# Performance work log

Hardware: AMD Instinct MI355X
Metric: run time of the kernel (lower is better)

The kernel has to match this reference:

```python
import jax, jax.numpy as jnp
import numpy as np

N_NODES = 100000
N_EDGES = 1600000
EMBED_DIM = 64


def setup_inputs() -> dict:
    key = jax.random.key(0)
    k_x, k_e, k_w, k_b = jax.random.split(key, 4)
    x = jax.random.normal(k_x, (N_NODES, EMBED_DIM), dtype=jnp.float32)
    edge_index = jax.random.randint(k_e, (2, N_EDGES), 0, N_NODES, dtype=jnp.int64)
    # nn.Linear(embed_dim, embed_dim): weight [out, in], bias [out]
    W = jax.random.normal(k_w, (EMBED_DIM, EMBED_DIM), dtype=jnp.float32) * (1.0 / np.sqrt(EMBED_DIM))
    b = jax.random.normal(k_b, (EMBED_DIM,), dtype=jnp.float32) * 0.01
    return {"x": x, "edge_index": edge_index, "W": W, "b": b, "num_node": N_NODES}


def reference(x, edge_index, W, b, num_node):
    source_nodes, target_nodes = edge_index[0], edge_index[1]
    # h = relu(Linear(x))  -> [N, d]
    h = jax.nn.relu(jnp.einsum("nd,od->no", x, W) + b)
    # gather messages at target nodes: [E, d]
    msgs = h[target_nodes]
    # scatter-add into source node slots (index_add_)
    aggr = jax.ops.segment_sum(msgs, source_nodes, num_segments=num_node)
    # mean normalization: bincount clamped to >= 1
    counts = jnp.bincount(source_nodes, length=num_node).astype(jnp.float32)
    counts = jnp.maximum(counts, 1.0)
    # dropout is identity at inference (training=False)
    return aggr / counts[:, None]
```

## Files before the change

### kernel.cpp

```cpp
#include <hip/hip_runtime.h>
#include <hip/hip_bf16.h>

#define DIM 64
#define SCAN_B 256
#define NXCD 8

__global__ void detect_layout_kernel(const int* __restrict__ ei32,
                                     int* __restrict__ flag) {
  int v = ei32[2 * threadIdx.x + 1];
  unsigned long long m = __ballot(v != 0);
  if (threadIdx.x == 0) *flag = (m == 0ULL) ? 1 : 0;
}

__device__ __forceinline__ int load_idx(const int* ei32, int is64, size_t pos) {
  return is64 ? ei32[2 * pos] : ei32[pos];
}

__global__ __launch_bounds__(256) void linear_relu_kernel(
    const float* __restrict__ x, const float* __restrict__ W,
    const float* __restrict__ b, float* __restrict__ h, int N) {
  __shared__ float Ws[DIM * DIM];
  __shared__ float bs[DIM];
  for (int i = threadIdx.x; i < DIM * DIM; i += 256) Ws[i] = W[i];
  if (threadIdx.x < DIM) bs[threadIdx.x] = b[threadIdx.x];
  __syncthreads();

  int row = blockIdx.x * 256 + threadIdx.x;
  if (row >= N) return;

  const float4* xr = (const float4*)(x + (size_t)row * DIM);
  float acc[DIM];
#pragma unroll
  for (int o = 0; o < DIM; ++o) acc[o] = bs[o];

#pragma unroll
  for (int i4 = 0; i4 < DIM / 4; ++i4) {
    float4 xv = xr[i4];
#pragma unroll
    for (int o = 0; o < DIM; ++o) {
      const float* wrow = &Ws[o * DIM + i4 * 4];
      acc[o] = fmaf(xv.x, wrow[0], acc[o]);
      acc[o] = fmaf(xv.y, wrow[1], acc[o]);
      acc[o] = fmaf(xv.z, wrow[2], acc[o]);
      acc[o] = fmaf(xv.w, wrow[3], acc[o]);
    }
  }

  float4* hr = (float4*)(h + (size_t)row * DIM);
#pragma unroll
  for (int o4 = 0; o4 < DIM / 4; ++o4) {
    float4 v;
    v.x = fmaxf(acc[o4 * 4 + 0], 0.0f);
    v.y = fmaxf(acc[o4 * 4 + 1], 0.0f);
    v.z = fmaxf(acc[o4 * 4 + 2], 0.0f);
    v.w = fmaxf(acc[o4 * 4 + 3], 0.0f);
    hr[o4] = v;
  }
}

__global__ __launch_bounds__(256) void hist_xcd_kernel(
    const int* __restrict__ ei32, const int* __restrict__ flag,
    int* __restrict__ counts8, int* __restrict__ rank,
    int* __restrict__ chunk_xcd, int N, int E) {
  unsigned int xcc;
  asm volatile("s_getreg_b32 %0, hwreg(HW_REG_XCC_ID)" : "=s"(xcc));
  xcc &= (NXCD - 1);
  if (threadIdx.x == 0) chunk_xcd[blockIdx.x] = (int)xcc;

  int e = blockIdx.x * 256 + threadIdx.x;
  if (e >= E) return;
  int src = load_idx(ei32, *flag, (size_t)e);
  int* ctr = counts8 + (size_t)xcc * N + src;
  int r = __hip_atomic_fetch_add(ctr, 1, __ATOMIC_RELAXED,
                                 __HIP_MEMORY_SCOPE_WORKGROUP);
  __builtin_nontemporal_store(r, &rank[e]);
}

__global__ void scan1_kernel(int* __restrict__ counts8, int* __restrict__ ctot,
                             int* __restrict__ offsets,
                             int* __restrict__ partials, int N) {
  __shared__ int s[SCAN_B];
  int t = threadIdx.x;
  int i = blockIdx.x * SCAN_B + t;
  int total = 0;
  if (i < N) {
    int run = 0;
#pragma unroll
    for (int x = 0; x < NXCD; ++x) {
      size_t idx = (size_t)x * N + i;
      int c = counts8[idx];
      counts8[idx] = run;
      run += c;
    }
    total = run;
    ctot[i] = total;
  }
  s[t] = total;
  __syncthreads();
  for (int off = 1; off < SCAN_B; off <<= 1) {
    int add = (t >= off) ? s[t - off] : 0;
    __syncthreads();
    s[t] += add;
    __syncthreads();
  }
  if (i < N) offsets[i] = s[t] - total;
  if (t == SCAN_B - 1) partials[blockIdx.x] = s[t];
}

__global__ void scan2_kernel(int* __restrict__ partials, int nb) {
  __shared__ int s[512];
  int t = threadIdx.x;
  int v = (t < nb) ? partials[t] : 0;
  s[t] = v;
  __syncthreads();
  for (int off = 1; off < 512; off <<= 1) {
    int add = (t >= off) ? s[t - off] : 0;
    __syncthreads();
    s[t] += add;
    __syncthreads();
  }
  if (t < nb) partials[t] = s[t] - v;
}

__global__ void scan3_kernel(int* __restrict__ offsets,
                             const int* __restrict__ partials, int N) {
  int i = blockIdx.x * SCAN_B + threadIdx.x;
  if (i < N) offsets[i] += partials[blockIdx.x];
}

__global__ __launch_bounds__(256) void place_kernel(
    const int* __restrict__ ei32, const int* __restrict__ flag,
    const int* __restrict__ offsets, const int* __restrict__ counts8,
    const int* __restrict__ rank, const int* __restrict__ chunk_xcd,
    int* __restrict__ bucket, int N, int E) {
  int e = blockIdx.x * 256 + threadIdx.x;
  if (e >= E) return;
  int is64 = *flag;
  int xcd = chunk_xcd[blockIdx.x];
  int src = load_idx(ei32, is64, (size_t)e);
  int tgt = load_idx(ei32, is64, (size_t)E + e);
  int r = __builtin_nontemporal_load(&rank[e]);
  int pos = offsets[src] + counts8[(size_t)xcd * N + src] + r;
  bucket[pos] = tgt;
}

__global__ __launch_bounds__(256) void gather_kernel(
    const float* __restrict__ h, const int* __restrict__ offsets,
    const int* __restrict__ ctot, const int* __restrict__ bucket,
    float* __restrict__ out, int N) {
  int wid = (blockIdx.x * 256 + threadIdx.x) >> 6;
  int lane = threadIdx.x & 63;
  if (wid >= N) return;

  int deg = ctot[wid];
  int start = offsets[wid];
  float a0 = 0.f, a1 = 0.f, a2 = 0.f, a3 = 0.f;
  float a4 = 0.f, a5 = 0.f, a6 = 0.f, a7 = 0.f;

  for (int j0 = 0; j0 < deg; j0 += 64) {
    int m = min(deg - j0, 64);
    int t = (lane < m) ? __builtin_nontemporal_load(&bucket[start + j0 + lane])
                       : 0;
    int j = 0;
    for (; j + 8 <= m; j += 8) {
      int t0 = __shfl(t, j);
      int t1 = __shfl(t, j + 1);
      int t2 = __shfl(t, j + 2);
      int t3 = __shfl(t, j + 3);
      int t4 = __shfl(t, j + 4);
      int t5 = __shfl(t, j + 5);
      int t6 = __shfl(t, j + 6);
      int t7 = __shfl(t, j + 7);
      float v0 = h[(size_t)t0 * DIM + lane];
      float v1 = h[(size_t)t1 * DIM + lane];
      float v2 = h[(size_t)t2 * DIM + lane];
      float v3 = h[(size_t)t3 * DIM + lane];
      float v4 = h[(size_t)t4 * DIM + lane];
      float v5 = h[(size_t)t5 * DIM + lane];
      float v6 = h[(size_t)t6 * DIM + lane];
      float v7 = h[(size_t)t7 * DIM + lane];
      a0 += v0; a1 += v1; a2 += v2; a3 += v3;
      a4 += v4; a5 += v5; a6 += v6; a7 += v7;
    }
    for (; j < m; ++j) {
      int tj = __shfl(t, j);
      a0 += h[(size_t)tj * DIM + lane];
    }
  }

  float c = (float)max(deg, 1);
  float acc = ((a0 + a1) + (a2 + a3)) + ((a4 + a5) + (a6 + a7));
  __builtin_nontemporal_store(acc / c, &out[(size_t)wid * DIM + lane]);
}

extern "C" void kernel_launch(void* const* d_in, const int* in_sizes, int n_in,
                              void* d_out, int out_size, void* d_ws, size_t ws_size,
                              hipStream_t stream) {
  const float* x = (const float*)d_in[0];
  const int* ei32 = (const int*)d_in[1];
  const float* W = (const float*)d_in[2];
  const float* b = (const float*)d_in[3];

  const int N = in_sizes[0] / DIM;
  const int E = in_sizes[1] / 2;

  float* out = (float*)d_out;
  int* rank = (int*)d_out;

  const int eb = (E + 255) / 256;
  char* p = (char*)d_ws;
  int* bucket = (int*)p;    p += (size_t)E * 4;
  int* counts8 = (int*)p;   p += (size_t)NXCD * N * 4;
  int* ctot = (int*)p;      p += (size_t)N * 4;
  int* offsets = (int*)p;   p += (size_t)N * 4;
  int* partials = (int*)p;  p += 512 * 4;
  int* flag = (int*)p;      p += 16;
  int* chunk_xcd = (int*)p; p += (size_t)eb * 4;
  p = (char*)(((uintptr_t)p + 15) & ~(uintptr_t)15);
  float* h = (float*)p;

  const int nb1 = (N + SCAN_B - 1) / SCAN_B;

  hipMemsetAsync(counts8, 0, (size_t)NXCD * N * 4, stream);

  detect_layout_kernel<<<1, 64, 0, stream>>>(ei32, flag);

  linear_relu_kernel<<<(N + 255) / 256, 256, 0, stream>>>(x, W, b, h, N);

  hist_xcd_kernel<<<eb, 256, 0, stream>>>(ei32, flag, counts8, rank,
                                          chunk_xcd, N, E);

  scan1_kernel<<<nb1, SCAN_B, 0, stream>>>(counts8, ctot, offsets, partials, N);
  scan2_kernel<<<1, 512, 0, stream>>>(partials, nb1);
  scan3_kernel<<<nb1, SCAN_B, 0, stream>>>(offsets, partials, N);

  place_kernel<<<eb, 256, 0, stream>>>(ei32, flag, offsets, counts8, rank,
                                       chunk_xcd, bucket, N, E);

  gather_kernel<<<(N * 64 + 255) / 256, 256, 0, stream>>>(h, offsets, ctot,
                                                          bucket, out, N);
}
```

Before: 321.6 us.

## Store h in fp16 and merge linear and histogram into one launch

The intermediate activation h is now written as fp16 instead of fp32, which halves the bytes the random-access gather reads per edge. The linear+ReLU kernel and the per-XCD source histogram kernel are merged into one grid, with block index choosing the role, so they run concurrently and one launch is removed. The cost is reduced precision in the messages (fp16 rounding before fp32 accumulation) and a shared-memory allocation in histogram blocks that they never use.

```diff
diff --git a/kernel.cpp b/kernel.cpp
--- a/kernel.cpp
+++ b/kernel.cpp
@@ -1,5 +1,6 @@
 #include <hip/hip_runtime.h>
 #include <hip/hip_bf16.h>
+#include <hip/hip_fp16.h>
 
 #define DIM 64
 #define SCAN_B 256
@@ -16,11 +17,33 @@
   return is64 ? ei32[2 * pos] : ei32[pos];
 }
 
-__global__ __launch_bounds__(256) void linear_relu_kernel(
+__global__ __launch_bounds__(256) void lin_hist_kernel(
     const float* __restrict__ x, const float* __restrict__ W,
-    const float* __restrict__ b, float* __restrict__ h, int N) {
+    const float* __restrict__ b, __half* __restrict__ h, int N, int nbLin,
+    const int* __restrict__ ei32, const int* __restrict__ flag,
+    int* __restrict__ counts8, int* __restrict__ rank,
+    int* __restrict__ chunk_xcd, int E) {
   __shared__ float Ws[DIM * DIM];
   __shared__ float bs[DIM];
+
+  if (blockIdx.x >= nbLin) {
+    unsigned int xcc;
+    asm volatile("s_getreg_b32 %0, hwreg(HW_REG_XCC_ID)" : "=s"(xcc));
+    xcc &= (NXCD - 1);
+    int c = blockIdx.x - nbLin;
+    if (threadIdx.x == 0) chunk_xcd[c] = (int)xcc;
+
+    int e = c * 256 + threadIdx.x;
+    if (e < E) {
+      int src = load_idx(ei32, *flag, (size_t)e);
+      int* ctr = counts8 + (size_t)xcc * N + src;
+      int r = __hip_atomic_fetch_add(ctr, 1, __ATOMIC_RELAXED,
+                                     __HIP_MEMORY_SCOPE_WORKGROUP);
+      __builtin_nontemporal_store(r, &rank[e]);
+    }
+    return;
+  }
+
   for (int i = threadIdx.x; i < DIM * DIM; i += 256) Ws[i] = W[i];
   if (threadIdx.x < DIM) bs[threadIdx.x] = b[threadIdx.x];
   __syncthreads();
@@ -46,34 +69,16 @@
     }
   }
 
-  float4* hr = (float4*)(h + (size_t)row * DIM);
+  ushort4* hr = (ushort4*)(h + (size_t)row * DIM);
 #pragma unroll
   for (int o4 = 0; o4 < DIM / 4; ++o4) {
-    float4 v;
-    v.x = fmaxf(acc[o4 * 4 + 0], 0.0f);
-    v.y = fmaxf(acc[o4 * 4 + 1], 0.0f);
-    v.z = fmaxf(acc[o4 * 4 + 2], 0.0f);
-    v.w = fmaxf(acc[o4 * 4 + 3], 0.0f);
+    ushort4 v;
+    v.x = __half_as_ushort(__float2half(fmaxf(acc[o4 * 4 + 0], 0.0f)));
+    v.y = __half_as_ushort(__float2half(fmaxf(acc[o4 * 4 + 1], 0.0f)));
+    v.z = __half_as_ushort(__float2half(fmaxf(acc[o4 * 4 + 2], 0.0f)));
+    v.w = __half_as_ushort(__float2half(fmaxf(acc[o4 * 4 + 3], 0.0f)));
     hr[o4] = v;
   }
-}
-
-__global__ __launch_bounds__(256) void hist_xcd_kernel(
-    const int* __restrict__ ei32, const int* __restrict__ flag,
-    int* __restrict__ counts8, int* __restrict__ rank,
-    int* __restrict__ chunk_xcd, int N, int E) {
-  unsigned int xcc;
-  asm volatile("s_getreg_b32 %0, hwreg(HW_REG_XCC_ID)" : "=s"(xcc));
-  xcc &= (NXCD - 1);
-  if (threadIdx.x == 0) chunk_xcd[blockIdx.x] = (int)xcc;
-
-  int e = blockIdx.x * 256 + threadIdx.x;
-  if (e >= E) return;
-  int src = load_idx(ei32, *flag, (size_t)e);
-  int* ctr = counts8 + (size_t)xcc * N + src;
-  int r = __hip_atomic_fetch_add(ctr, 1, __ATOMIC_RELAXED,
-                                 __HIP_MEMORY_SCOPE_WORKGROUP);
-  __builtin_nontemporal_store(r, &rank[e]);
 }
 
 __global__ void scan1_kernel(int* __restrict__ counts8, int* __restrict__ ctot,
@@ -86,8 +91,8 @@
   if (i < N) {
     int run = 0;
 #pragma unroll
-    for (int x = 0; x < NXCD; ++x) {
-      size_t idx = (size_t)x * N + i;
+    for (int xx = 0; xx < NXCD; ++xx) {
+      size_t idx = (size_t)xx * N + i;
       int c = counts8[idx];
       counts8[idx] = run;
       run += c;
@@ -140,12 +145,11 @@
   int src = load_idx(ei32, is64, (size_t)e);
   int tgt = load_idx(ei32, is64, (size_t)E + e);
   int r = __builtin_nontemporal_load(&rank[e]);
-  int pos = offsets[src] + counts8[(size_t)xcd * N + src] + r;
-  bucket[pos] = tgt;
+  bucket[offsets[src] + counts8[(size_t)xcd * N + src] + r] = tgt;
 }
 
 __global__ __launch_bounds__(256) void gather_kernel(
-    const float* __restrict__ h, const int* __restrict__ offsets,
+    const __half* __restrict__ h, const int* __restrict__ offsets,
     const int* __restrict__ ctot, const int* __restrict__ bucket,
     float* __restrict__ out, int N) {
   int wid = (blockIdx.x * 256 + threadIdx.x) >> 6;
@@ -171,20 +175,20 @@
       int t5 = __shfl(t, j + 5);
       int t6 = __shfl(t, j + 6);
       int t7 = __shfl(t, j + 7);
-      float v0 = h[(size_t)t0 * DIM + lane];
-      float v1 = h[(size_t)t1 * DIM + lane];
-      float v2 = h[(size_t)t2 * DIM + lane];
-      float v3 = h[(size_t)t3 * DIM + lane];
-      float v4 = h[(size_t)t4 * DIM + lane];
-      float v5 = h[(size_t)t5 * DIM + lane];
-      float v6 = h[(size_t)t6 * DIM + lane];
-      float v7 = h[(size_t)t7 * DIM + lane];
+      float v0 = __half2float(h[(size_t)t0 * DIM + lane]);
+      float v1 = __half2float(h[(size_t)t1 * DIM + lane]);
+      float v2 = __half2float(h[(size_t)t2 * DIM + lane]);
+      float v3 = __half2float(h[(size_t)t3 * DIM + lane]);
+      float v4 = __half2float(h[(size_t)t4 * DIM + lane]);
+      float v5 = __half2float(h[(size_t)t5 * DIM + lane]);
+      float v6 = __half2float(h[(size_t)t6 * DIM + lane]);
+      float v7 = __half2float(h[(size_t)t7 * DIM + lane]);
       a0 += v0; a1 += v1; a2 += v2; a3 += v3;
       a4 += v4; a5 += v5; a6 += v6; a7 += v7;
     }
     for (; j < m; ++j) {
       int tj = __shfl(t, j);
-      a0 += h[(size_t)tj * DIM + lane];
+      a0 += __half2float(h[(size_t)tj * DIM + lane]);
     }
   }
 
@@ -217,18 +221,18 @@
   int* flag = (int*)p;      p += 16;
   int* chunk_xcd = (int*)p; p += (size_t)eb * 4;
   p = (char*)(((uintptr_t)p + 15) & ~(uintptr_t)15);
-  float* h = (float*)p;
+  __half* h = (__half*)p;
 
   const int nb1 = (N + SCAN_B - 1) / SCAN_B;
+  const int nbLin = (N + 255) / 256;
 
   hipMemsetAsync(counts8, 0, (size_t)NXCD * N * 4, stream);
 
   detect_layout_kernel<<<1, 64, 0, stream>>>(ei32, flag);
 
-  linear_relu_kernel<<<(N + 255) / 256, 256, 0, stream>>>(x, W, b, h, N);
-
-  hist_xcd_kernel<<<eb, 256, 0, stream>>>(ei32, flag, counts8, rank,
-                                          chunk_xcd, N, E);
+  lin_hist_kernel<<<nbLin + eb, 256, 0, stream>>>(x, W, b, h, N, nbLin, ei32,
+                                                  flag, counts8, rank,
+                                                  chunk_xcd, E);
 
   scan1_kernel<<<nb1, SCAN_B, 0, stream>>>(counts8, ctot, offsets, partials, N);
   scan2_kernel<<<1, 512, 0, stream>>>(partials, nb1);
```

Result: faster. 281.9 us (-12.4%).
